# Kernel optimization log

Hardware: AMD Instinct MI355X
Metric: run time of the kernel (lower is better)

The kernel has to match this reference:

```python
import jax, jax.numpy as jnp
import numpy as np

B, T, D, H, K, DEPTH = 2, 2048, 512, 8, 16, 3
EPS = 1e-5


def setup_inputs() -> dict:
    key = jax.random.key(0)
    ks = jax.random.split(key, 6)
    s = 0.02
    return {
        "x": jax.random.normal(ks[0], (B, T, D), jnp.float32),
        "ln1_s": jnp.ones((DEPTH, D), jnp.float32),
        "ln1_b": jnp.zeros((DEPTH, D), jnp.float32),
        "qkv_w": jax.random.normal(ks[1], (DEPTH, D, 3 * D), jnp.float32) * s,
        "proj_w": jax.random.normal(ks[2], (DEPTH, D, D), jnp.float32) * s,
        "proj_b": jnp.zeros((DEPTH, D), jnp.float32),
        "ln2_s": jnp.ones((DEPTH, D), jnp.float32),
        "ln2_b": jnp.zeros((DEPTH, D), jnp.float32),
        "w1": jax.random.normal(ks[3], (DEPTH, D, 4 * D), jnp.float32) * s,
        "b1": jnp.zeros((DEPTH, 4 * D), jnp.float32),
        "w2": jax.random.normal(ks[4], (DEPTH, 4 * D, D), jnp.float32) * s,
        "b2": jnp.zeros((DEPTH, D), jnp.float32),
    }


def _ln(x, s, b):
    m = x.mean(-1, keepdims=True)
    v = ((x - m) ** 2).mean(-1, keepdims=True)
    return (x - m) * jax.lax.rsqrt(v + EPS) * s + b


def _dilated_mask(t, dil):
    # allowed key j for query i: j = i - step*dil, step in [0, K), j >= 0
    i = jnp.arange(t)[:, None]
    j = jnp.arange(t)[None, :]
    diff = i - j
    ok = (diff >= 0) & (diff % dil == 0) & (diff < K * dil)
    return jnp.where(ok, 0.0, -jnp.inf).astype(jnp.float32)


def reference(x, ln1_s, ln1_b, qkv_w, proj_w, proj_b, ln2_s, ln2_b, w1, b1, w2, b2):
    hd = D // H
    scale = hd ** -0.5
    for d in range(DEPTH):
        dil = 2 ** d
        h = _ln(x, ln1_s[d], ln1_b[d])
        qkv = (h @ qkv_w[d]).reshape(B, T, 3, H, hd).transpose(2, 0, 3, 1, 4)
        q, k, v = qkv[0], qkv[1], qkv[2]  # each (B,H,T,hd)
        attn = jnp.einsum('bhid,bhjd->bhij', q, k) * scale + _dilated_mask(T, dil)
        o = jnp.einsum('bhij,bhjd->bhid', jax.nn.softmax(attn, axis=-1), v)
        o = o.transpose(0, 2, 1, 3).reshape(B, T, D) @ proj_w[d] + proj_b[d]
        x = x + o
        h = _ln(x, ln2_s[d], ln2_b[d])
        x = x + (jax.nn.gelu(h @ w1[d] + b1[d], approximate=False) @ w2[d] + b2[d])
    return x
```

## Files before the change

### kernel.cpp

```cpp
#include <hip/hip_runtime.h>
#include <math.h>

#define TSEQ   2048
#define DM     512
#define NH     8
#define HD     64
#define KATT   16
#define NDEPTH 3
#define MROWS  4096

typedef __attribute__((ext_vector_type(8))) short bf16x8;
typedef __attribute__((ext_vector_type(8))) unsigned short u16x8;
typedef __attribute__((ext_vector_type(4))) float f32x4;

static __device__ __forceinline__ unsigned short f2b(float f) {
    unsigned int u = __float_as_uint(f);
    unsigned int r = (u + 0x7fffu + ((u >> 16) & 1u)) >> 16;
    return (unsigned short)r;
}
static __device__ __forceinline__ float b2f(unsigned short s) {
    return __uint_as_float((unsigned int)s << 16);
}

static __device__ __forceinline__ void load_lds16(const void* g, void* l) {
    __builtin_amdgcn_global_load_lds(
        (const __attribute__((address_space(1))) unsigned int*)g,
        (__attribute__((address_space(3))) unsigned int*)l, 16, 0, 0);
}

static __device__ __forceinline__ float fast_erf(float x) {
    const float a  = fabsf(x);
    const float t  = 1.0f / (1.0f + 0.3275911f * a);
    const float p  = t * (0.254829592f + t * (-0.284496736f +
                     t * (1.421413741f + t * (-1.453152027f + t * 1.061405429f))));
    const float e  = __expf(-a * a);
    const float r  = 1.0f - p * e;
    return __builtin_copysignf(r, x);
}

__global__ __launch_bounds__(256) void prep_kernel(
    const float* __restrict__ qkv_w, const float* __restrict__ proj_w,
    const float* __restrict__ w1,    const float* __restrict__ w2,
    unsigned short* __restrict__ qkvT, unsigned short* __restrict__ projT,
    unsigned short* __restrict__ w1T,  unsigned short* __restrict__ w2T,
    const float* __restrict__ x, const float* __restrict__ sc,
    const float* __restrict__ bi, unsigned short* __restrict__ h)
{
    __shared__ float tile[32][33];
    int id = blockIdx.x;
    const int tid = threadIdx.x;

    if (id < 9216) {
        const float* W; unsigned short* Wt; int Kd, Nd;
        if (id < 2304)      { W = qkv_w;  Wt = qkvT;  Kd = 512;  Nd = 1536; }
        else if (id < 3072) { W = proj_w; Wt = projT; Kd = 512;  Nd = 512;  id -= 2304; }
        else if (id < 6144) { W = w1;     Wt = w1T;   Kd = 512;  Nd = 2048; id -= 3072; }
        else                { W = w2;     Wt = w2T;   Kd = 2048; Nd = 512;  id -= 6144; }
        const int nt = Nd >> 5, per = nt * (Kd >> 5);
        const int d = id / per, rem = id % per;
        const int k0 = (rem / nt) * 32, n0 = (rem % nt) * 32;

        const size_t off = (size_t)d * Kd * Nd;
        const float* Wd = W + off;
        unsigned short* Wtd = Wt + off;
        const int tx = tid & 31, ty = tid >> 5;
#pragma unroll
        for (int r = 0; r < 32; r += 8)
            tile[ty + r][tx] = Wd[(size_t)(k0 + ty + r) * Nd + (n0 + tx)];
        __syncthreads();
#pragma unroll
        for (int r = 0; r < 32; r += 8)
            Wtd[(size_t)(n0 + ty + r) * Kd + (k0 + tx)] = f2b(tile[tx][ty + r]);
        return;
    }

    const int wid  = (id - 9216) * 4 + (tid >> 6);
    const int lane = tid & 63;
    const float* xr = x + (size_t)wid * DM;
    const float4 v0 = *(const float4*)&xr[lane * 4];
    const float4 v1 = *(const float4*)&xr[256 + lane * 4];
    float s = v0.x + v0.y + v0.z + v0.w + v1.x + v1.y + v1.z + v1.w;
    float q = v0.x*v0.x + v0.y*v0.y + v0.z*v0.z + v0.w*v0.w
            + v1.x*v1.x + v1.y*v1.y + v1.z*v1.z + v1.w*v1.w;
#pragma unroll
    for (int off = 32; off; off >>= 1) {
        s += __shfl_xor(s, off, 64);
        q += __shfl_xor(q, off, 64);
    }
    const float mean = s * (1.0f / DM);
    const float var  = q * (1.0f / DM) - mean * mean;
    const float rs   = rsqrtf(var + 1e-5f);
    unsigned short* hr = h + (size_t)wid * DM;
    const int c0 = lane * 4, c1 = 256 + lane * 4;
    ushort4 o0, o1;
    o0.x = f2b((v0.x - mean) * rs * sc[c0+0] + bi[c0+0]);
    o0.y = f2b((v0.y - mean) * rs * sc[c0+1] + bi[c0+1]);
    o0.z = f2b((v0.z - mean) * rs * sc[c0+2] + bi[c0+2]);
    o0.w = f2b((v0.w - mean) * rs * sc[c0+3] + bi[c0+3]);
    o1.x = f2b((v1.x - mean) * rs * sc[c1+0] + bi[c1+0]);
    o1.y = f2b((v1.y - mean) * rs * sc[c1+1] + bi[c1+1]);
    o1.z = f2b((v1.z - mean) * rs * sc[c1+2] + bi[c1+2]);
    o1.w = f2b((v1.w - mean) * rs * sc[c1+3] + bi[c1+3]);
    *(ushort4*)&hr[c0] = o0;
    *(ushort4*)&hr[c1] = o1;
}

__global__ __launch_bounds__(256) void attn_kernel(
    const unsigned short* __restrict__ qh, const unsigned short* __restrict__ kh,
    const unsigned short* __restrict__ vh, unsigned short* __restrict__ o, int dil)
{
    const int nwg = gridDim.x;
    const int wg  = (blockIdx.x & 7) * (nwg >> 3) + (blockIdx.x >> 3);
    const int tile = wg & (TSEQ / 16 - 1);
    const int bh   = wg >> 7;
    const int b    = bh >> 3, hh = bh & 7;
    const int t0   = tile * 16;
    const int tid  = threadIdx.x;
    const int wave = tid >> 6, lane = tid & 63;
    const int tq   = wave * 4 + (lane >> 4);
    const int s    = lane & 15;
    const int t    = t0 + tq;
    const size_t slab = ((size_t)hh * MROWS + (size_t)b * TSEQ) * HD;

    const int R    = 15 * dil + 16;
    const int base = t0 - 15 * dil;

    __shared__ unsigned short ks[76 * 64];
    __shared__ unsigned short vs[76 * 64];
    __shared__ unsigned short qs[16 * 64];
    __shared__ float p_lds[16][17];

    for (int c = tid; c < R * 8; c += 256) {
        const int r = c >> 3, cs = c & 7;
        const int sr = max(base + r, 0);
        const int ps = ((cs + r + (r >> 2)) & 7) * 8;
        const size_t g = slab + (size_t)sr * HD + cs * 8;
        *(u16x8*)&ks[r * 64 + ps] = *(const u16x8*)(kh + g);
        *(u16x8*)&vs[r * 64 + ps] = *(const u16x8*)(vh + g);
    }
    if (tid < 128) {
        const int r = tid >> 3, cs = tid & 7;
        *(u16x8*)&qs[r * 64 + cs * 8] =
            *(const u16x8*)(qh + slab + (size_t)(t0 + r) * HD + cs * 8);
    }
    __syncthreads();

    const bool valid = (t - s * dil) >= 0;
    const int  kidx  = tq + 15 * dil - s * dil;
    float dot = 0.0f;
#pragma unroll
    for (int j = 0; j < 8; j++) {
        const u16x8 kk = *(const u16x8*)&ks[kidx * 64 + (((j + kidx + (kidx >> 2)) & 7) * 8)];
        const u16x8 qq = *(const u16x8*)&qs[tq * 64 + j * 8];
#pragma unroll
        for (int e = 0; e < 8; e++) dot += b2f(qq[e]) * b2f(kk[e]);
    }
    const float sc = valid ? dot * 0.125f : -1e30f;
    float m = sc;
#pragma unroll
    for (int off = 1; off < 16; off <<= 1) m = fmaxf(m, __shfl_xor(m, off, 64));
    const float p = expf(sc - m);
    float l = p;
#pragma unroll
    for (int off = 1; off < 16; off <<= 1) l += __shfl_xor(l, off, 64);
    p_lds[tq][s] = p / l;
    __syncthreads();

    const int dp  = lane & 31;
    const int qh2 = lane >> 5;
#pragma unroll
    for (int qi = 0; qi < 2; qi++) {
        const int qq = qi * 8 + wave * 2 + qh2;
        float a0 = 0.0f, a1 = 0.0f;
#pragma unroll
        for (int ss = 0; ss < KATT; ss++) {
            const int idx = qq + 15 * dil - ss * dil;
            const float pw = p_lds[qq][ss];
            const int ch = ((dp >> 2) + idx + (idx >> 2)) & 7;
            const unsigned int vv =
                *(const unsigned int*)&vs[idx * 64 + ch * 8 + (dp & 3) * 2];
            a0 += pw * b2f((unsigned short)(vv & 0xffffu));
            a1 += pw * b2f((unsigned short)(vv >> 16));
        }
        unsigned short* orow = o + (size_t)(b * TSEQ + (t0 + qq)) * DM + (size_t)hh * HD;
        const unsigned int packed = (unsigned int)f2b(a0) | ((unsigned int)f2b(a1) << 16);
        *(unsigned int*)&orow[dp * 2] = packed;
    }
}

template<int EPI, int TN, int PK>
__global__ __launch_bounds__(256) void gemm_kernel(
    const unsigned short* __restrict__ A,
    const unsigned short* __restrict__ Bt,
    const float* __restrict__ bias,
    unsigned short* __restrict__ outp,
    unsigned short* __restrict__ outb,
    unsigned short* __restrict__ outq,
    unsigned short* __restrict__ outk,
    unsigned short* __restrict__ outv,
    int N, int K, int Kslice, size_t zstride, int gx, int gy)
{
    constexpr int FN = TN / 32;
    constexpr int CA = 2;
    constexpr int CB = TN / 64;
    const int tid  = threadIdx.x;
    const int wave = tid >> 6, lane = tid & 63;

    const int nwg = gridDim.x;
    const int wg  = (blockIdx.x & 7) * (nwg >> 3) + (blockIdx.x >> 3);
    const int bxi = wg % gx;
    const int byi = (wg / gx) % gy;
    const int bzi = wg / (gx * gy);

    const int bm = byi * 128;
    const int bn = bxi * TN;
    const int wm = (wave >> 1) * 64;
    const int wn = (wave & 1) * (TN / 2);
    const int ml = lane & 15, quad = lane >> 4;
    const int kbeg = bzi * Kslice;

    __shared__ unsigned short As[2 * PK][128 * 32];
    __shared__ unsigned short Bs[2 * PK][TN * 32];

    f32x4 acc[4][FN] = {};

    const int rr = lane >> 2, ss = lane & 3;
    const int cc = ((ss - (rr >> 1)) & 3) * 8;
    const unsigned short* Aa[CA];
    const unsigned short* Bb[CB];
#pragma unroll
    for (int j = 0; j < CA; j++)
        Aa[j] = A + (size_t)(bm + (wave * CA + j) * 16 + rr) * K + kbeg + cc;
#pragma unroll
    for (int j = 0; j < CB; j++)
        Bb[j] = Bt + (size_t)(bn + (wave * CB + j) * 16 + rr) * K + kbeg + cc;

    const int fslot = ((quad + (ml >> 1)) & 3) * 8;

#pragma unroll
    for (int p = 0; p < PK; p++) {
#pragma unroll
        for (int j = 0; j < CA; j++)
            load_lds16(Aa[j] + p * 32, &As[p][(wave * CA + j) * 512]);
#pragma unroll
        for (int j = 0; j < CB; j++)
            load_lds16(Bb[j] + p * 32, &Bs[p][(wave * CB + j) * 512]);
    }
    __syncthreads();

    const int steps = Kslice / (32 * PK);
    for (int s = 0; s < steps; s++) {
        const int cb = (s & 1) * PK, nb = cb ^ PK;
        const bool more = (s + 1 < steps);
        if (more) {
#pragma unroll
            for (int p = 0; p < PK; p++) {
                const int k0 = ((s + 1) * PK + p) * 32;
#pragma unroll
                for (int j = 0; j < CA; j++)
                    load_lds16(Aa[j] + k0, &As[nb + p][(wave * CA + j) * 512]);
#pragma unroll
                for (int j = 0; j < CB; j++)
                    load_lds16(Bb[j] + k0, &Bs[nb + p][(wave * CB + j) * 512]);
            }
        }

#pragma unroll
        for (int p = 0; p < PK; p++) {
            bf16x8 af[4], bfr[FN];
#pragma unroll
            for (int i = 0; i < 4; i++)
                af[i] = *(const bf16x8*)&As[cb + p][(wm + i * 16 + ml) * 32 + fslot];
#pragma unroll
            for (int j = 0; j < FN; j++)
                bfr[j] = *(const bf16x8*)&Bs[cb + p][(wn + j * 16 + ml) * 32 + fslot];

#pragma unroll
            for (int i = 0; i < 4; i++)
#pragma unroll
                for (int j = 0; j < FN; j++)
                    acc[i][j] = __builtin_amdgcn_mfma_f32_16x16x32_bf16(
                        af[i], bfr[j], acc[i][j], 0, 0, 0);
        }

        if (more) __syncthreads();
    }

    unsigned short* op = outp + (size_t)bzi * zstride;
#pragma unroll
    for (int i = 0; i < 4; i++)
#pragma unroll
        for (int j = 0; j < FN; j++)
#pragma unroll
            for (int r = 0; r < 4; r++) {
                const int row = bm + wm + i * 16 + quad * 4 + r;
                const int col = bn + wn + j * 16 + ml;
                const float v = acc[i][j][r];
                if (EPI == 0) {
                    op[(size_t)row * N + col] = f2b(v);
                } else if (EPI == 2) {
                    const float u = v + bias[col];
                    const float g = 0.5f * u * (1.0f + fast_erf(u * 0.70710678118654752f));
                    outb[(size_t)row * N + col] = f2b(g);
                } else {
                    const int which = col >> 9;
                    const int hh = (col & 511) >> 6;
                    const int dim = col & 63;
                    unsigned short* dst =
                        which == 0 ? outq : (which == 1 ? outk : outv);
                    dst[((size_t)hh * MROWS + row) * HD + dim] = f2b(v);
                }
            }
}

template<bool DO_LN, int Z>
__global__ __launch_bounds__(256) void reduce_kernel(
    const float* __restrict__ xin,
    const unsigned short* __restrict__ part,
    const float* __restrict__ bias,
    const float* __restrict__ lns, const float* __restrict__ lnb,
    float* __restrict__ xout, unsigned short* __restrict__ h)
{
    const int wid  = blockIdx.x * 4 + (threadIdx.x >> 6);
    const int lane = threadIdx.x & 63;
    const int c0 = lane * 4, c1 = 256 + lane * 4;
    const size_t ro = (size_t)wid * DM;

    float4 a0 = *(const float4*)&xin[ro + c0];
    float4 a1 = *(const float4*)&xin[ro + c1];
#pragma unroll
    for (int z = 0; z < Z; z++) {
        const unsigned short* p = part + (size_t)z * (MROWS * (size_t)DM) + ro;
        const ushort4 p0 = *(const ushort4*)&p[c0];
        const ushort4 p1 = *(const ushort4*)&p[c1];
        a0.x += b2f(p0.x); a0.y += b2f(p0.y); a0.z += b2f(p0.z); a0.w += b2f(p0.w);
        a1.x += b2f(p1.x); a1.y += b2f(p1.y); a1.z += b2f(p1.z); a1.w += b2f(p1.w);
    }
    a0.x += bias[c0+0]; a0.y += bias[c0+1]; a0.z += bias[c0+2]; a0.w += bias[c0+3];
    a1.x += bias[c1+0]; a1.y += bias[c1+1]; a1.z += bias[c1+2]; a1.w += bias[c1+3];

    *(float4*)&xout[ro + c0] = a0;
    *(float4*)&xout[ro + c1] = a1;

    if (DO_LN) {
        float s = a0.x + a0.y + a0.z + a0.w + a1.x + a1.y + a1.z + a1.w;
        float q = a0.x*a0.x + a0.y*a0.y + a0.z*a0.z + a0.w*a0.w
                + a1.x*a1.x + a1.y*a1.y + a1.z*a1.z + a1.w*a1.w;
#pragma unroll
        for (int off = 32; off; off >>= 1) {
            s += __shfl_xor(s, off, 64);
            q += __shfl_xor(q, off, 64);
        }
        const float mean = s * (1.0f / DM);
        const float var  = q * (1.0f / DM) - mean * mean;
        const float rs   = rsqrtf(var + 1e-5f);
        unsigned short* hr = h + ro;
        ushort4 o0, o1;
        o0.x = f2b((a0.x - mean) * rs * lns[c0+0] + lnb[c0+0]);
        o0.y = f2b((a0.y - mean) * rs * lns[c0+1] + lnb[c0+1]);
        o0.z = f2b((a0.z - mean) * rs * lns[c0+2] + lnb[c0+2]);
        o0.w = f2b((a0.w - mean) * rs * lns[c0+3] + lnb[c0+3]);
        o1.x = f2b((a1.x - mean) * rs * lns[c1+0] + lnb[c1+0]);
        o1.y = f2b((a1.y - mean) * rs * lns[c1+1] + lnb[c1+1]);
        o1.z = f2b((a1.z - mean) * rs * lns[c1+2] + lnb[c1+2]);
        o1.w = f2b((a1.w - mean) * rs * lns[c1+3] + lnb[c1+3]);
        *(ushort4*)&hr[c0] = o0;
        *(ushort4*)&hr[c1] = o1;
    }
}

extern "C" void kernel_launch(void* const* d_in, const int* in_sizes, int n_in,
                              void* d_out, int out_size, void* d_ws, size_t ws_size,
                              hipStream_t stream)
{
    (void)in_sizes; (void)n_in; (void)out_size; (void)ws_size;
    const float* x_in   = (const float*)d_in[0];
    const float* ln1_s  = (const float*)d_in[1];
    const float* ln1_b  = (const float*)d_in[2];
    const float* qkv_w  = (const float*)d_in[3];
    const float* proj_w = (const float*)d_in[4];
    const float* proj_b = (const float*)d_in[5];
    const float* ln2_s  = (const float*)d_in[6];
    const float* ln2_b  = (const float*)d_in[7];
    const float* w1     = (const float*)d_in[8];
    const float* b1     = (const float*)d_in[9];
    const float* w2     = (const float*)d_in[10];
    const float* b2     = (const float*)d_in[11];

    char* ws = (char*)d_ws;
    float*          xbuf = (float*)(ws);
    unsigned short* qhb  = (unsigned short*)(ws + 8388608);
    unsigned short* khb  = (unsigned short*)(ws + 12582912);
    unsigned short* vhb  = (unsigned short*)(ws + 16777216);
    unsigned short* ubuf = (unsigned short*)(ws + 33554432);
    unsigned short* hbuf = (unsigned short*)(ws + 50331648);
    unsigned short* obuf = (unsigned short*)(ws + 54525952);
    unsigned short* part = (unsigned short*)(ws + 58720256);
    unsigned short* qkvT = (unsigned short*)(ws + 92274688);
    unsigned short* projT= (unsigned short*)(ws + 96993280);
    unsigned short* w1T  = (unsigned short*)(ws + 98566144);
    unsigned short* w2T  = (unsigned short*)(ws + 104857600);

    const size_t ZS = (size_t)MROWS * DM;

    prep_kernel<<<10240, 256, 0, stream>>>(
        qkv_w, proj_w, w1, w2, qkvT, projT, w1T, w2T,
        x_in, ln1_s, ln1_b, hbuf);

    for (int d = 0; d < NDEPTH; d++) {
        const int dil = 1 << d;
        const float* xin = (d == 0) ? x_in : xbuf;

        gemm_kernel<3, 64, 2><<<768, 256, 0, stream>>>(
            hbuf, qkvT + (size_t)d * 1536 * 512, nullptr, nullptr, nullptr,
            qhb, khb, vhb, 1536, 512, 512, 0, 24, 32);
        attn_kernel<<<2 * NH * (TSEQ / 16), 256, 0, stream>>>(qhb, khb, vhb, obuf, dil);
        gemm_kernel<0, 64, 2><<<512, 256, 0, stream>>>(
            obuf, projT + (size_t)d * 512 * 512, nullptr, part, nullptr,
            nullptr, nullptr, nullptr, 512, 512, 256, ZS, 8, 32);
        reduce_kernel<true, 2><<<MROWS / 4, 256, 0, stream>>>(
            xin, part, proj_b + d * DM, ln2_s + d * DM, ln2_b + d * DM,
            xbuf, hbuf);
        gemm_kernel<2, 64, 1><<<1024, 256, 0, stream>>>(
            hbuf, w1T + (size_t)d * 2048 * 512, b1 + d * 2048, nullptr, ubuf,
            nullptr, nullptr, nullptr, 2048, 512, 512, 0, 32, 32);
        gemm_kernel<0, 64, 1><<<1024, 256, 0, stream>>>(
            ubuf, w2T + (size_t)d * 512 * 2048, nullptr, part, nullptr,
            nullptr, nullptr, nullptr, 512, 2048, 512, ZS, 8, 32);
        if (d < NDEPTH - 1) {
            reduce_kernel<true, 4><<<MROWS / 4, 256, 0, stream>>>(
                xbuf, part, b2 + d * DM, ln1_s + (d+1) * DM, ln1_b + (d+1) * DM,
                xbuf, hbuf);
        } else {
            reduce_kernel<false, 4><<<MROWS / 4, 256, 0, stream>>>(
                xbuf, part, b2 + d * DM, nullptr, nullptr,
                (float*)d_out, nullptr);
        }
    }
}
```

Measured before the change: 357.2 us.

## Triple-buffer GEMM LDS pipeline with explicit vmcnt waits and two-stage prefetch

Replaces the double-buffered GEMM main loop, which used a PK k-chunk template parameter, with a three-slot LDS ring. Global-to-LDS loads are issued two K-steps ahead, and each step waits with a hand-written s_waitcnt vmcnt that leaves the newest stage in flight, followed by a raw s_barrier. The aim is to keep memory loads overlapping MFMA work instead of draining every load at each __syncthreads. In exchange it uses more LDS per block and needs a barrier every 32-wide K step. It also depends on load_lds16 being counted by vmcnt and on the hard-coded wait counts matching the number of loads per stage.

```diff
diff --git a/kernel.cpp b/kernel.cpp
--- a/kernel.cpp
+++ b/kernel.cpp
@@ -188,7 +188,7 @@
     }
 }
 
-template<int EPI, int TN, int PK>
+template<int EPI, int TN>
 __global__ __launch_bounds__(256) void gemm_kernel(
     const unsigned short* __restrict__ A,
     const unsigned short* __restrict__ Bt,
@@ -203,6 +203,7 @@
     constexpr int FN = TN / 32;
     constexpr int CA = 2;
     constexpr int CB = TN / 64;
+    constexpr int L  = CA + CB;
     const int tid  = threadIdx.x;
     const int wave = tid >> 6, lane = tid & 63;
 
@@ -219,8 +220,8 @@
     const int ml = lane & 15, quad = lane >> 4;
     const int kbeg = bzi * Kslice;
 
-    __shared__ unsigned short As[2 * PK][128 * 32];
-    __shared__ unsigned short Bs[2 * PK][TN * 32];
+    __shared__ unsigned short As[3][128 * 32];
+    __shared__ unsigned short Bs[3][TN * 32];
 
     f32x4 acc[4][FN] = {};
 
@@ -238,52 +239,60 @@
     const int fslot = ((quad + (ml >> 1)) & 3) * 8;
 
 #pragma unroll
-    for (int p = 0; p < PK; p++) {
-#pragma unroll
-        for (int j = 0; j < CA; j++)
-            load_lds16(Aa[j] + p * 32, &As[p][(wave * CA + j) * 512]);
-#pragma unroll
-        for (int j = 0; j < CB; j++)
-            load_lds16(Bb[j] + p * 32, &Bs[p][(wave * CB + j) * 512]);
-    }
-    __syncthreads();
-
-    const int steps = Kslice / (32 * PK);
+    for (int j = 0; j < CA; j++) load_lds16(Aa[j],      &As[0][(wave * CA + j) * 512]);
+#pragma unroll
+    for (int j = 0; j < CB; j++) load_lds16(Bb[j],      &Bs[0][(wave * CB + j) * 512]);
+#pragma unroll
+    for (int j = 0; j < CA; j++) load_lds16(Aa[j] + 32, &As[1][(wave * CA + j) * 512]);
+#pragma unroll
+    for (int j = 0; j < CB; j++) load_lds16(Bb[j] + 32, &Bs[1][(wave * CB + j) * 512]);
+    __builtin_amdgcn_sched_barrier(0);
+    if constexpr (L == 3) asm volatile("s_waitcnt vmcnt(3)" ::: "memory");
+    else                  asm volatile("s_waitcnt vmcnt(4)" ::: "memory");
+    __builtin_amdgcn_s_barrier();
+    __builtin_amdgcn_sched_barrier(0);
+
+    const int steps = Kslice >> 5;
+    int cur = 0;
     for (int s = 0; s < steps; s++) {
-        const int cb = (s & 1) * PK, nb = cb ^ PK;
-        const bool more = (s + 1 < steps);
-        if (more) {
-#pragma unroll
-            for (int p = 0; p < PK; p++) {
-                const int k0 = ((s + 1) * PK + p) * 32;
-#pragma unroll
-                for (int j = 0; j < CA; j++)
-                    load_lds16(Aa[j] + k0, &As[nb + p][(wave * CA + j) * 512]);
-#pragma unroll
-                for (int j = 0; j < CB; j++)
-                    load_lds16(Bb[j] + k0, &Bs[nb + p][(wave * CB + j) * 512]);
+        const int nx2 = (cur == 0) ? 2 : (cur - 1);
+        if (s + 2 < steps) {
+            const int k0 = (s + 2) * 32;
+#pragma unroll
+            for (int j = 0; j < CA; j++)
+                load_lds16(Aa[j] + k0, &As[nx2][(wave * CA + j) * 512]);
+#pragma unroll
+            for (int j = 0; j < CB; j++)
+                load_lds16(Bb[j] + k0, &Bs[nx2][(wave * CB + j) * 512]);
+        }
+
+        bf16x8 af[4], bfr[FN];
+#pragma unroll
+        for (int i = 0; i < 4; i++)
+            af[i] = *(const bf16x8*)&As[cur][(wm + i * 16 + ml) * 32 + fslot];
+#pragma unroll
+        for (int j = 0; j < FN; j++)
+            bfr[j] = *(const bf16x8*)&Bs[cur][(wn + j * 16 + ml) * 32 + fslot];
+
+#pragma unroll
+        for (int i = 0; i < 4; i++)
+#pragma unroll
+            for (int j = 0; j < FN; j++)
+                acc[i][j] = __builtin_amdgcn_mfma_f32_16x16x32_bf16(
+                    af[i], bfr[j], acc[i][j], 0, 0, 0);
+
+        if (s + 1 < steps) {
+            __builtin_amdgcn_sched_barrier(0);
+            if (s + 2 < steps) {
+                if constexpr (L == 3) asm volatile("s_waitcnt vmcnt(3)" ::: "memory");
+                else                  asm volatile("s_waitcnt vmcnt(4)" ::: "memory");
+            } else {
+                asm volatile("s_waitcnt vmcnt(0)" ::: "memory");
             }
+            __builtin_amdgcn_s_barrier();
+            __builtin_amdgcn_sched_barrier(0);
         }
-
-#pragma unroll
-        for (int p = 0; p < PK; p++) {
-            bf16x8 af[4], bfr[FN];
-#pragma unroll
-            for (int i = 0; i < 4; i++)
-                af[i] = *(const bf16x8*)&As[cb + p][(wm + i * 16 + ml) * 32 + fslot];
-#pragma unroll
-            for (int j = 0; j < FN; j++)
-                bfr[j] = *(const bf16x8*)&Bs[cb + p][(wn + j * 16 + ml) * 32 + fslot];
-
-#pragma unroll
-            for (int i = 0; i < 4; i++)
-#pragma unroll
-                for (int j = 0; j < FN; j++)
-                    acc[i][j] = __builtin_amdgcn_mfma_f32_16x16x32_bf16(
-                        af[i], bfr[j], acc[i][j], 0, 0, 0);
-        }
-
-        if (more) __syncthreads();
+        cur = (cur == 2) ? 0 : (cur + 1);
     }
 
     unsigned short* op = outp + (size_t)bzi * zstride;
@@ -411,20 +420,20 @@
         const int dil = 1 << d;
         const float* xin = (d == 0) ? x_in : xbuf;
 
-        gemm_kernel<3, 64, 2><<<768, 256, 0, stream>>>(
+        gemm_kernel<3, 64><<<768, 256, 0, stream>>>(
             hbuf, qkvT + (size_t)d * 1536 * 512, nullptr, nullptr, nullptr,
             qhb, khb, vhb, 1536, 512, 512, 0, 24, 32);
         attn_kernel<<<2 * NH * (TSEQ / 16), 256, 0, stream>>>(qhb, khb, vhb, obuf, dil);
-        gemm_kernel<0, 64, 2><<<512, 256, 0, stream>>>(
+        gemm_kernel<0, 64><<<512, 256, 0, stream>>>(
             obuf, projT + (size_t)d * 512 * 512, nullptr, part, nullptr,
             nullptr, nullptr, nullptr, 512, 512, 256, ZS, 8, 32);
         reduce_kernel<true, 2><<<MROWS / 4, 256, 0, stream>>>(
             xin, part, proj_b + d * DM, ln2_s + d * DM, ln2_b + d * DM,
             xbuf, hbuf);
-        gemm_kernel<2, 64, 1><<<1024, 256, 0, stream>>>(
+        gemm_kernel<2, 64><<<1024, 256, 0, stream>>>(
             hbuf, w1T + (size_t)d * 2048 * 512, b1 + d * 2048, nullptr, ubuf,
             nullptr, nullptr, nullptr, 2048, 512, 512, 0, 32, 32);
-        gemm_kernel<0, 64, 1><<<1024, 256, 0, stream>>>(
+        gemm_kernel<0, 64><<<1024, 256, 0, stream>>>(
             ubuf, w2T + (size_t)d * 512 * 2048, nullptr, part, nullptr,
             nullptr, nullptr, nullptr, 512, 2048, 512, ZS, 8, 32);
         if (d < NDEPTH - 1) {
```

Measured after the change: 368.3 us. +3.1%, slower.
